# Optimization experiments

Measured on AMD Instinct MI355X. Metric: run time of the kernel, lower is better.

Reference implementation:

```python
import jax, jax.numpy as jnp
import numpy as np

X_DIM, Z_DIM, N_HEIGHT = 256, 256, 32
EPS = 1e-5  # BatchNorm1d eps

def _bn(x, g, b):
    # BatchNorm1d in training mode: batch statistics over the point axis
    m = x.mean(0)
    v = x.var(0)
    return (x - m) * jax.lax.rsqrt(v + EPS) * g + b

def setup_inputs() -> dict:
    key = jax.random.key(0)
    ks = jax.random.split(key, 16)
    B, N, F = 2, 120000, 3
    inp = {
        'pt_fea': jax.random.normal(ks[0], (B, N, F), jnp.float32),
        'grid_ind': jax.random.randint(ks[1], (B, N, 2), 0, 256, dtype=jnp.int32).astype(jnp.int64),
        'occupancy': (jax.random.uniform(ks[2], (B, 1, X_DIM, N_HEIGHT, Z_DIM)) < 0.1).astype(jnp.float32),
    }
    dims = [(3, 64), (64, 128), (128, 256), (256, 512)]
    for i, (di, do) in enumerate(dims):
        inp[f'W{i+1}'] = jax.random.normal(ks[3 + i], (di, do), jnp.float32) * 0.02
        inp[f'b{i+1}'] = jnp.zeros((do,), jnp.float32)
    for i, d in enumerate([3, 64, 128, 256]):
        inp[f'g{i}'] = jnp.ones((d,), jnp.float32)
        inp[f'be{i}'] = jnp.zeros((d,), jnp.float32)
    inp['Wc'] = jax.random.normal(ks[10], (512, 32), jnp.float32) * 0.02
    inp['bc'] = jnp.zeros((32,), jnp.float32)
    return inp

def reference(pt_fea, occupancy, W1, b1, W2, b2, W3, b3, W4, b4,
              g0, be0, g1, be1, g2, be2, g3, be3, Wc, bc, grid_ind):
    B, N, F = pt_fea.shape
    feats = pt_fea.reshape(B * N, F)                          # cat over batch
    # PointNet per-point MLP: BN -> (Linear -> BN -> ReLU) x3 -> Linear
    h = _bn(feats, g0, be0)
    h = jax.nn.relu(_bn(h @ W1 + b1, g1, be1))
    h = jax.nn.relu(_bn(h @ W2 + b2, g2, be2))
    h = jax.nn.relu(_bn(h @ W3 + b3, g3, be3))
    h = h @ W4 + b4                                           # [B*N, 512]

    # linear segment id per (batch, x, z) cell; equivalent to unique+scatter_max
    gi = grid_ind.reshape(B * N, 2).astype(jnp.int32)
    batch_idx = jnp.repeat(jnp.arange(B, dtype=jnp.int32), N)
    seg = batch_idx * (X_DIM * Z_DIM) + gi[:, 0] * Z_DIM + gi[:, 1]
    n_cells = B * X_DIM * Z_DIM

    pooled = jax.ops.segment_max(h, seg, num_segments=n_cells)          # [cells, 512]
    cnt = jax.ops.segment_sum(jnp.ones((B * N,), h.dtype), seg, num_segments=n_cells)
    occ_mask = (cnt > 0)[:, None]
    pooled = jnp.where(occ_mask, pooled, 0.0)                           # kill -inf empties

    # feature compression on occupied cells only; empty cells stay exactly 0
    comp = jax.nn.relu(pooled @ Wc + bc)
    comp = jnp.where(occ_mask, comp, 0.0)                               # [cells, 32]

    bev = comp.reshape(B, X_DIM, Z_DIM, -1).transpose(0, 3, 1, 2)       # [B, 32, X, Z]
    # MaxPool2d(k=3, stride=1, pad=1); -inf padding matches torch's implicit -inf pad
    bev = jax.lax.reduce_window(bev, -jnp.inf, jax.lax.max,
                                (1, 1, 3, 3), (1, 1, 1, 1), 'SAME')

    occu = occupancy[:, 0].transpose(0, 2, 1, 3)                        # [B, H, X, Z]
    out = jnp.concatenate([occu, bev], axis=1)                          # [B, H+32, X, Z]
    return out
```

## Files before the change

### kernel.cpp

```cpp
#include <hip/hip_runtime.h>
#include <hip/hip_bf16.h>

#define EPSN 1e-5f

typedef __bf16 bf16x8 __attribute__((ext_vector_type(8)));
typedef float f32x4 __attribute__((ext_vector_type(4)));

__device__ __forceinline__ unsigned encf(float f) {
  unsigned u = __float_as_uint(f);
  return (u & 0x80000000u) ? ~u : (u | 0x80000000u);
}
__device__ __forceinline__ float decf(unsigned u) {
  return (u & 0x80000000u) ? __uint_as_float(u ^ 0x80000000u) : __uint_as_float(~u);
}

__global__ __launch_bounds__(256) void stats_feats(const float* __restrict__ pt, int n,
                                                   float* __restrict__ sums) {
  float a0 = 0, a1 = 0, a2 = 0, q0 = 0, q1 = 0, q2 = 0;
  for (int p = blockIdx.x * 256 + threadIdx.x; p < n; p += gridDim.x * 256) {
    float v0 = pt[3 * p], v1 = pt[3 * p + 1], v2 = pt[3 * p + 2];
    a0 += v0; a1 += v1; a2 += v2;
    q0 += v0 * v0; q1 += v1 * v1; q2 += v2 * v2;
  }
  __shared__ float red[4][6];
  float vals[6] = {a0, a1, a2, q0, q1, q2};
  int lane = threadIdx.x & 63, wv = threadIdx.x >> 6;
#pragma unroll
  for (int k = 0; k < 6; k++) {
    float v = vals[k];
#pragma unroll
    for (int o = 32; o; o >>= 1) v += __shfl_down(v, o, 64);
    if (lane == 0) red[wv][k] = v;
  }
  __syncthreads();
  if (threadIdx.x < 6) {
    float v = red[0][threadIdx.x] + red[1][threadIdx.x] + red[2][threadIdx.x] + red[3][threadIdx.x];
    atomicAdd(&sums[threadIdx.x], v);
  }
}

__global__ void bn_prep(const float* __restrict__ sums, int C, float invN,
                        const float* __restrict__ g, const float* __restrict__ be,
                        float* __restrict__ sc, float* __restrict__ sh) {
  int c = threadIdx.x;
  if (c < C) {
    float m = sums[c] * invN;
    float v = fmaxf(sums[C + c] * invN - m * m, 0.f);
    float s = g[c] * rsqrtf(v + EPSN);
    sc[c] = s;
    sh[c] = be[c] - m * s;
  }
}

__global__ __launch_bounds__(256) void wconv(const float* __restrict__ W,
                                             __hip_bfloat16* __restrict__ Wt, int K, int C) {
  int idx = blockIdx.x * 256 + threadIdx.x;
  if (idx >= K * C) return;
  int k = idx / C, c = idx - k * C;
  Wt[(size_t)c * K + k] = __float2bfloat16(W[idx]);
}

__global__ __launch_bounds__(256) void gemm1_stats(const float* __restrict__ pt,
                                                   const float* __restrict__ W,
                                                   const float* __restrict__ bias,
                                                   const float* __restrict__ scsh,
                                                   __hip_bfloat16* __restrict__ Y,
                                                   int n, float* __restrict__ sums) {
  const int c = threadIdx.x & 63;
  const float w0 = W[c], w1 = W[64 + c], w2 = W[128 + c], bb = bias[c];
  const float s0 = scsh[0], s1 = scsh[1], s2 = scsh[2];
  const float h0 = scsh[4], h1 = scsh[5], h2 = scsh[6];
  float s = 0.f, q = 0.f;
  const int total = n * 64;
  for (int idx = blockIdx.x * 256 + threadIdx.x; idx < total; idx += gridDim.x * 256) {
    int p = idx >> 6;
    float x0 = s0 * pt[3 * p]     + h0;
    float x1 = s1 * pt[3 * p + 1] + h1;
    float x2 = s2 * pt[3 * p + 2] + h2;
    float y = bb + x0 * w0 + x1 * w1 + x2 * w2;
    Y[idx] = __float2bfloat16(y);
    s += y; q += y * y;
  }
  __shared__ float sred[4][64], qred[4][64];
  int wv = threadIdx.x >> 6;
  sred[wv][c] = s; qred[wv][c] = q;
  __syncthreads();
  if (threadIdx.x < 64) {
    float S = sred[0][c] + sred[1][c] + sred[2][c] + sred[3][c];
    float Q = qred[0][c] + qred[1][c] + qred[2][c] + qred[3][c];
    atomicAdd(&sums[c], S);
    atomicAdd(&sums[64 + c], Q);
  }
}

template <int K>
__global__ __launch_bounds__(256) void gemm_mfma(
    const __hip_bfloat16* __restrict__ Yin, const __hip_bfloat16* __restrict__ Wt,
    const float* __restrict__ bias, const float* __restrict__ sc, const float* __restrict__ sh,
    __hip_bfloat16* __restrict__ Yout, int C, float* __restrict__ sums, int nrows) {
  constexpr int KS = 64, LDA = 72, LDO = 80;
  __shared__ __align__(16) __hip_bfloat16 hA[128 * LDO];
  __shared__ float sredArr[128], qredArr[128];
  const int t = threadIdx.x;
  const int lane = t & 63, wv = t >> 6;
  const int mh = (wv >> 1) * 64, nh = (wv & 1) * 64;
  const int lm = lane & 15, lq = lane >> 4;
  const int p0 = blockIdx.x * 128;
  const int cb0 = blockIdx.y * 128;

  f32x4 acc[4][4];
#pragma unroll
  for (int i = 0; i < 4; i++)
#pragma unroll
    for (int j = 0; j < 4; j++) acc[i][j] = {0.f, 0.f, 0.f, 0.f};

  for (int k0 = 0; k0 < K; k0 += KS) {
    __syncthreads();
#pragma unroll
    for (int it = 0; it < 4; it++) {
      int idx = it * 256 + t;
      int row = idx >> 3;
      int c8 = (idx & 7) * 8;
      int gp = p0 + row;
      __hip_bfloat16 h8[8];
      if (gp < nrows) {
        uint4 raw = *(const uint4*)(Yin + (size_t)gp * K + k0 + c8);
        const __hip_bfloat16* pr = (const __hip_bfloat16*)&raw;
#pragma unroll
        for (int j = 0; j < 8; j++) {
          float v = sc[k0 + c8 + j] * __bfloat162float(pr[j]) + sh[k0 + c8 + j];
          h8[j] = __float2bfloat16(fmaxf(v, 0.f));
        }
      } else {
#pragma unroll
        for (int j = 0; j < 8; j++) h8[j] = __float2bfloat16(0.f);
      }
      *(uint4*)&hA[row * LDA + c8] = *(const uint4*)h8;
    }
    __syncthreads();
#pragma unroll
    for (int kk = 0; kk < KS; kk += 32) {
      bf16x8 a[4], b[4];
#pragma unroll
      for (int i = 0; i < 4; i++)
        a[i] = *(const bf16x8*)&hA[(mh + i * 16 + lm) * LDA + kk + lq * 8];
#pragma unroll
      for (int j = 0; j < 4; j++)
        b[j] = *(const bf16x8*)(const void*)(Wt + (size_t)(cb0 + nh + j * 16 + lm) * K + k0 + kk + lq * 8);
#pragma unroll
      for (int i = 0; i < 4; i++)
#pragma unroll
        for (int j = 0; j < 4; j++)
          acc[i][j] = __builtin_amdgcn_mfma_f32_16x16x32_bf16(a[i], b[j], acc[i][j], 0, 0, 0);
    }
  }

#pragma unroll
  for (int j = 0; j < 4; j++) {
    float bb = bias[cb0 + nh + j * 16 + lm];
#pragma unroll
    for (int i = 0; i < 4; i++)
#pragma unroll
      for (int r = 0; r < 4; r++) acc[i][j][r] += bb;
  }

  __syncthreads();
  if (t < 128) { sredArr[t] = 0.f; qredArr[t] = 0.f; }
  __syncthreads();

#pragma unroll
  for (int j = 0; j < 4; j++) {
    float s = 0.f, q = 0.f;
#pragma unroll
    for (int i = 0; i < 4; i++)
#pragma unroll
      for (int r = 0; r < 4; r++) {
        int grow = p0 + mh + i * 16 + lq * 4 + r;
        if (grow < nrows) { float v = acc[i][j][r]; s += v; q += v * v; }
      }
    s += __shfl_xor(s, 16); s += __shfl_xor(s, 32);
    q += __shfl_xor(q, 16); q += __shfl_xor(q, 32);
    if (lq == 0) {
      atomicAdd(&sredArr[nh + j * 16 + lm], s);
      atomicAdd(&qredArr[nh + j * 16 + lm], q);
    }
  }

  for (int half = 0; half < 2; half++) {
    __syncthreads();
    if ((wv & 1) == half) {
#pragma unroll
      for (int j = 0; j < 4; j++)
#pragma unroll
        for (int i = 0; i < 4; i++)
#pragma unroll
          for (int r = 0; r < 4; r++)
            hA[(mh + i * 16 + lq * 4 + r) * LDO + j * 16 + lm] = __float2bfloat16(acc[i][j][r]);
    }
    __syncthreads();
    int row = t >> 1, seg = t & 1;
    if (p0 + row < nrows) {
      const uint4* src = (const uint4*)&hA[row * LDO + seg * 32];
      uint4* dst = (uint4*)(Yout + (size_t)(p0 + row) * C + cb0 + half * 64 + seg * 32);
      dst[0] = src[0]; dst[1] = src[1]; dst[2] = src[2]; dst[3] = src[3];
    }
  }

  if (t < 128) {
    atomicAdd(&sums[cb0 + t], sredArr[t]);
    atomicAdd(&sums[C + cb0 + t], qredArr[t]);
  }
}

__global__ __launch_bounds__(256) void hist_kernel(const int* __restrict__ gi, int perB,
                                                   unsigned* __restrict__ hist) {
  int b = blockIdx.y;
  int p = blockIdx.x * 256 + threadIdx.x;
  if (p < perB) {
    int gp = b * perB + p;
    int c = (gi[2 * gp] & 255) * 256 + (gi[2 * gp + 1] & 255);
    atomicAdd(&hist[b * 65536 + c], 1u);
  }
}
__global__ __launch_bounds__(256) void scan1(const unsigned* __restrict__ hist,
                                             unsigned* __restrict__ cursor,
                                             unsigned* __restrict__ bSums) {
  __shared__ unsigned s[256];
  int b = blockIdx.y;
  int t = threadIdx.x, i = b * 65536 + blockIdx.x * 256 + t;
  unsigned v = hist[i]; s[t] = v; __syncthreads();
  for (int off = 1; off < 256; off <<= 1) {
    unsigned x = (t >= off) ? s[t - off] : 0u; __syncthreads();
    s[t] += x; __syncthreads();
  }
  cursor[i] = s[t] - v;
  if (t == 255) bSums[b * 256 + blockIdx.x] = s[255];
}
__global__ void scan2(unsigned* __restrict__ bSums) {
  __shared__ unsigned s[256];
  int t = threadIdx.x, i = blockIdx.x * 256 + t;
  unsigned v = bSums[i]; s[t] = v; __syncthreads();
  for (int off = 1; off < 256; off <<= 1) {
    unsigned x = (t >= off) ? s[t - off] : 0u; __syncthreads();
    s[t] += x; __syncthreads();
  }
  bSums[i] = s[t] - v;
}
__global__ __launch_bounds__(256) void mk_starts(const unsigned* __restrict__ cursor,
                                                 const unsigned* __restrict__ bSums,
                                                 unsigned* __restrict__ starts, int perB) {
  int b = blockIdx.y;
  int i = blockIdx.x * 256 + threadIdx.x;
  starts[b * 65537 + i] = cursor[b * 65536 + i] + bSums[b * 256 + (i >> 8)];
  if (i == 0) starts[b * 65537 + 65536] = (unsigned)perB;
}
__global__ __launch_bounds__(256) void scatter_kernel(const int* __restrict__ gi, int perB,
                                                      unsigned* __restrict__ cursor,
                                                      const unsigned* __restrict__ bSums,
                                                      unsigned* __restrict__ sorted,
                                                      unsigned* __restrict__ cells) {
  int b = blockIdx.y;
  int p = blockIdx.x * 256 + threadIdx.x;
  if (p < perB) {
    int gp = b * perB + p;
    int c = (gi[2 * gp] & 255) * 256 + (gi[2 * gp + 1] & 255);
    unsigned pos = atomicAdd(&cursor[b * 65536 + c], 1u) + bSums[b * 256 + (c >> 8)];
    if (pos < (unsigned)perB) {
      sorted[b * perB + pos] = (unsigned)p;
      cells[b * perB + pos] = (unsigned)c;
    }
  }
}

__global__ __launch_bounds__(256, 2) void pool_compress(
    const __hip_bfloat16* __restrict__ Y3, const __hip_bfloat16* __restrict__ Wt4,
    const float* __restrict__ b4, const float* __restrict__ sc, const float* __restrict__ sh,
    const __hip_bfloat16* __restrict__ WcT, const float* __restrict__ bc,
    const unsigned* __restrict__ sortedIdx, const unsigned* __restrict__ sortedCell,
    const unsigned* __restrict__ startsAll, float* __restrict__ comp, int perB) {
  constexpr int K = 256, KS = 64, LDA = 72, MLW = 129, NC = 40;
  __shared__ __align__(16) __hip_bfloat16 hA[128 * LDA];
  __shared__ __align__(16) unsigned maxLds[48 * MLW];
  __shared__ unsigned char slotRow[128];
  __shared__ int rowIdxLds[128];
  const int t = threadIdx.x;
  const int lane = t & 63, wv = t >> 6;
  const int lm = lane & 15, lq = lane >> 4;
  const int mh = (wv >> 1) * 64, nh = (wv & 1) * 64;
  const int batch = blockIdx.y;
  const unsigned* starts = startsAll + batch * 65537;
  const int c0 = blockIdx.x * NC;
  const int cEnd = min(c0 + NC, 65536);
  const int r0 = (int)starts[c0];
  int n = (int)starts[cEnd] - r0;
  if (n > 128) n = 128;
  if (n < 0) n = 0;

  if (t < 128) {
    if (t < n) {
      rowIdxLds[t] = (int)sortedIdx[batch * perB + r0 + t] + batch * perB;
      slotRow[t] = (unsigned char)((sortedCell[batch * perB + r0 + t] - c0) % NC);
    } else {
      rowIdxLds[t] = 0;
      slotRow[t] = 0;
    }
  }

  f32x4 accC[2];
  accC[0] = {0.f, 0.f, 0.f, 0.f};
  accC[1] = {0.f, 0.f, 0.f, 0.f};

#pragma unroll
  for (int half = 0; half < 2; half++) {
    f32x4 acc[2][4][4];
#pragma unroll
    for (int s2 = 0; s2 < 2; s2++)
#pragma unroll
      for (int i = 0; i < 4; i++)
#pragma unroll
        for (int j = 0; j < 4; j++) acc[s2][i][j] = {0.f, 0.f, 0.f, 0.f};

    for (int k0 = 0; k0 < K; k0 += KS) {
      __syncthreads();
#pragma unroll
      for (int it = 0; it < 4; it++) {
        int idx = it * 256 + t;
        int row = idx >> 3;
        int c8 = (idx & 7) * 8;
        __hip_bfloat16 h8[8];
        if (row < n) {
          uint4 raw = *(const uint4*)(Y3 + (size_t)rowIdxLds[row] * K + k0 + c8);
          const __hip_bfloat16* pr = (const __hip_bfloat16*)&raw;
#pragma unroll
          for (int j = 0; j < 8; j++) {
            float v = sc[k0 + c8 + j] * __bfloat162float(pr[j]) + sh[k0 + c8 + j];
            h8[j] = __float2bfloat16(fmaxf(v, 0.f));
          }
        } else {
#pragma unroll
          for (int j = 0; j < 8; j++) h8[j] = __float2bfloat16(0.f);
        }
        *(uint4*)&hA[row * LDA + c8] = *(const uint4*)h8;
      }
      __syncthreads();
#pragma unroll
      for (int kk = 0; kk < KS; kk += 32) {
        bf16x8 a[4];
#pragma unroll
        for (int i = 0; i < 4; i++)
          a[i] = *(const bf16x8*)&hA[(mh + i * 16 + lm) * LDA + kk + lq * 8];
#pragma unroll
        for (int s2 = 0; s2 < 2; s2++) {
          bf16x8 b[4];
#pragma unroll
          for (int j = 0; j < 4; j++)
            b[j] = *(const bf16x8*)(const void*)(Wt4 + (size_t)(half * 256 + s2 * 128 + nh + j * 16 + lm) * K + k0 + kk + lq * 8);
#pragma unroll
          for (int i = 0; i < 4; i++)
#pragma unroll
            for (int j = 0; j < 4; j++)
              acc[s2][i][j] = __builtin_amdgcn_mfma_f32_16x16x32_bf16(a[i], b[j], acc[s2][i][j], 0, 0, 0);
        }
      }
    }

#pragma unroll
    for (int s2 = 0; s2 < 2; s2++) {
      const int cc = half * 2 + s2;
      __syncthreads();
      for (int i = t; i < 48 * MLW; i += 256) maxLds[i] = 0u;
      __syncthreads();
#pragma unroll
      for (int j = 0; j < 4; j++) {
        int colq = nh + j * 16 + lm;
        float bb = b4[cc * 128 + colq];
#pragma unroll
        for (int i = 0; i < 4; i++) {
#pragma unroll
          for (int r = 0; r < 4; r++) {
            int lrow = mh + i * 16 + lq * 4 + r;
            if (lrow < n)
              atomicMax(&maxLds[(int)slotRow[lrow] * MLW + colq], encf(acc[s2][i][j][r] + bb));
          }
        }
      }
      __syncthreads();
      if (wv < 3) {
#pragma unroll
        for (int ks = 0; ks < 4; ks++) {
          int koff = ks * 32 + lq * 8;
          uint4 m0 = *(const uint4*)&maxLds[(wv * 16 + lm) * MLW + koff];
          uint4 m1 = *(const uint4*)&maxLds[(wv * 16 + lm) * MLW + koff + 4];
          unsigned mu[8] = {m0.x, m0.y, m0.z, m0.w, m1.x, m1.y, m1.z, m1.w};
          __hip_bfloat16 af[8];
#pragma unroll
          for (int j = 0; j < 8; j++) af[j] = __float2bfloat16(decf(mu[j]));
          bf16x8 a = *(const bf16x8*)af;
#pragma unroll
          for (int jn = 0; jn < 2; jn++) {
            bf16x8 b = *(const bf16x8*)(const void*)(WcT + (size_t)(jn * 16 + lm) * 512 + cc * 128 + koff);
            accC[jn] = __builtin_amdgcn_mfma_f32_16x16x32_bf16(a, b, accC[jn], 0, 0, 0);
          }
        }
      }
    }
  }
  if (wv < 3) {
#pragma unroll
    for (int jn = 0; jn < 2; jn++) {
      float bb = bc[jn * 16 + lm];
#pragma unroll
      for (int r = 0; r < 4; r++) {
        int cell = c0 + wv * 16 + lq * 4 + r;
        if (cell < cEnd) {
          int occ = starts[cell + 1] > starts[cell];
          float v = occ ? fmaxf(accC[jn][r] + bb, 0.f) : 0.f;
          comp[((size_t)batch * 65536 + cell) * 32 + jn * 16 + lm] = v;
        }
      }
    }
  }
}

__global__ __launch_bounds__(256) void maxpool_write(const float* __restrict__ comp,
                                                     float* __restrict__ out) {
  __shared__ float tile[32][65];
  int bid = blockIdx.x;
  int z0 = (bid & 3) * 64, x = (bid >> 2) & 255, b = bid >> 10;
  int f = threadIdx.x & 31, zs = threadIdx.x >> 5;
  for (int zi = 0; zi < 8; zi++) {
    int z = z0 + zi * 8 + zs;
    float m = -3.402823466e38f;
    for (int dx = -1; dx <= 1; dx++) {
      int xx = x + dx;
      if (xx < 0 || xx > 255) continue;
      for (int dz = -1; dz <= 1; dz++) {
        int zz = z + dz;
        if (zz < 0 || zz > 255) continue;
        m = fmaxf(m, comp[(size_t)((b << 16) + (xx << 8) + zz) * 32 + f]);
      }
    }
    tile[f][zi * 8 + zs] = m;
  }
  __syncthreads();
  int f2 = threadIdx.x >> 3, seg = threadIdx.x & 7;
  float* dst = out + ((size_t)(b * 64 + 32 + f2) * 256 + x) * 256 + z0 + seg * 8;
#pragma unroll
  for (int u = 0; u < 8; u++) dst[u] = tile[f2][seg * 8 + u];
}

__global__ __launch_bounds__(256) void occu_write(const float* __restrict__ occ,
                                                  float* __restrict__ out) {
  int idx = blockIdx.x * 256 + threadIdx.x;
  int z = idx & 255, x = (idx >> 8) & 255, hh = (idx >> 16) & 31, b = idx >> 21;
  out[((size_t)(b * 64 + hh) * 256 + x) * 256 + z] =
      occ[((size_t)((b * 256 + x) * 32 + hh)) * 256 + z];
}

extern "C" void kernel_launch(void* const* d_in, const int* in_sizes, int n_in,
                              void* d_out, int out_size, void* d_ws, size_t ws_size,
                              hipStream_t stream) {
  const float* pt_fea   = (const float*)d_in[0];
  const int*   grid_ind = (const int*)d_in[1];
  const float* occup    = (const float*)d_in[2];
  const float* W1 = (const float*)d_in[3];  const float* b1 = (const float*)d_in[4];
  const float* W2 = (const float*)d_in[5];  const float* b2 = (const float*)d_in[6];
  const float* W3 = (const float*)d_in[7];  const float* b3 = (const float*)d_in[8];
  const float* W4 = (const float*)d_in[9];  const float* b4 = (const float*)d_in[10];
  const float* g0 = (const float*)d_in[11]; const float* be0 = (const float*)d_in[12];
  const float* g1 = (const float*)d_in[13]; const float* be1 = (const float*)d_in[14];
  const float* g2 = (const float*)d_in[15]; const float* be2 = (const float*)d_in[16];
  const float* g3 = (const float*)d_in[17]; const float* be3 = (const float*)d_in[18];
  const float* Wc = (const float*)d_in[19]; const float* bc = (const float*)d_in[20];
  float* out = (float*)d_out;

  const int nPts = in_sizes[0] / 3;
  const int perB = nPts / 2;
  const float invN = 1.f / (float)nPts;

  char* ws = (char*)d_ws;
  float* stats = (float*)ws;
  float* scsh  = (float*)(ws + 4096);
  float* sums0 = stats;        float* sums1 = stats + 16;
  float* sums2 = stats + 160;  float* sums3 = stats + 416;
  float* sc0 = scsh;
  float* sc1 = scsh + 16;   float* sh1 = scsh + 80;
  float* sc2 = scsh + 144;  float* sh2 = scsh + 272;
  float* sc3 = scsh + 400;  float* sh3 = scsh + 656;
  __hip_bfloat16* Wt2 = (__hip_bfloat16*)(ws + 8192);
  __hip_bfloat16* Wt3 = (__hip_bfloat16*)(ws + 24576);
  __hip_bfloat16* Wt4 = (__hip_bfloat16*)(ws + 90112);
  __hip_bfloat16* WcT = (__hip_bfloat16*)(ws + 352256);
  char* S0 = ws + 385024;
  __hip_bfloat16* Y1 = (__hip_bfloat16*)S0;
  __hip_bfloat16* Y2 = (__hip_bfloat16*)(S0 + 30720000ll);
  __hip_bfloat16* Y3 = (__hip_bfloat16*)(S0 + 92160000ll);
  float* comp       = (float*)S0;
  char* sortBase    = S0 + 16777216ll;
  unsigned* hist    = (unsigned*)sortBase;
  unsigned* cursor  = hist + 2 * 65536;
  unsigned* bSums   = cursor + 2 * 65536;
  unsigned* startsA = bSums + 1024;
  unsigned* sorted  = startsA + 131080;
  unsigned* cells   = sorted + 2 * perB;

  hipMemsetAsync(stats, 0, 4096, stream);

  wconv<<<(64 * 128 + 255) / 256, 256, 0, stream>>>(W2, Wt2, 64, 128);
  wconv<<<(128 * 256 + 255) / 256, 256, 0, stream>>>(W3, Wt3, 128, 256);
  wconv<<<(256 * 512 + 255) / 256, 256, 0, stream>>>(W4, Wt4, 256, 512);
  wconv<<<(512 * 32 + 255) / 256, 256, 0, stream>>>(Wc, WcT, 512, 32);

  stats_feats<<<256, 256, 0, stream>>>(pt_fea, nPts, sums0);
  bn_prep<<<1, 256, 0, stream>>>(sums0, 3, invN, g0, be0, sc0, scsh + 4);

  gemm1_stats<<<512, 256, 0, stream>>>(pt_fea, W1, b1, scsh, Y1, nPts, sums1);
  bn_prep<<<1, 256, 0, stream>>>(sums1, 64, invN, g1, be1, sc1, sh1);

  gemm_mfma<64><<<dim3(nPts / 128, 1), 256, 0, stream>>>(Y1, Wt2, b2, sc1, sh1, Y2, 128, sums2, nPts);
  bn_prep<<<1, 256, 0, stream>>>(sums2, 128, invN, g2, be2, sc2, sh2);

  gemm_mfma<128><<<dim3(nPts / 128, 2), 256, 0, stream>>>(Y2, Wt3, b3, sc2, sh2, Y3, 256, sums3, nPts);
  bn_prep<<<1, 256, 0, stream>>>(sums3, 256, invN, g3, be3, sc3, sh3);

  hipMemsetAsync(hist, 0, 2 * 65536 * 4, stream);
  const int pgrid = (perB + 255) / 256;
  hist_kernel<<<dim3(pgrid, 2), 256, 0, stream>>>(grid_ind, perB, hist);
  scan1<<<dim3(256, 2), 256, 0, stream>>>(hist, cursor, bSums);
  scan2<<<2, 256, 0, stream>>>(bSums);
  mk_starts<<<dim3(256, 2), 256, 0, stream>>>(cursor, bSums, startsA, perB);
  scatter_kernel<<<dim3(pgrid, 2), 256, 0, stream>>>(grid_ind, perB, cursor, bSums, sorted, cells);

  pool_compress<<<dim3((65536 + 39) / 40, 2), 256, 0, stream>>>(
      Y3, Wt4, b4, sc3, sh3, WcT, bc, sorted, cells, startsA, comp, perB);

  maxpool_write<<<2048, 256, 0, stream>>>(comp, out);
  occu_write<<<16384, 256, 0, stream>>>(occup, out);
}
```

Before: 830.6 us.

## Sort points by cell before the MLP so pooling reads Y3 contiguously

Moves the counting sort ahead of the MLP. The first layer gathers input points in sorted order, so every later activation buffer is already cell-ordered and pool_compress reads Y3 rows contiguously instead of through an index indirection. Slot assignment is rebuilt from the starts array instead of a per-point cells buffer, MFMA and atomic work is skipped for fully empty 16-row tiles, and the occupancy hint is raised to 3 blocks per CU. The trade-off is a gather in gemm1 and aliasing the sorted buffer into Y2 scratch space, which makes buffer lifetimes more fragile.

```diff
diff --git a/kernel.cpp b/kernel.cpp
--- a/kernel.cpp
+++ b/kernel.cpp
@@ -64,8 +64,9 @@
                                                    const float* __restrict__ W,
                                                    const float* __restrict__ bias,
                                                    const float* __restrict__ scsh,
+                                                   const unsigned* __restrict__ sorted,
                                                    __hip_bfloat16* __restrict__ Y,
-                                                   int n, float* __restrict__ sums) {
+                                                   int n, int perB, float* __restrict__ sums) {
   const int c = threadIdx.x & 63;
   const float w0 = W[c], w1 = W[64 + c], w2 = W[128 + c], bb = bias[c];
   const float s0 = scsh[0], s1 = scsh[1], s2 = scsh[2];
@@ -73,10 +74,11 @@
   float s = 0.f, q = 0.f;
   const int total = n * 64;
   for (int idx = blockIdx.x * 256 + threadIdx.x; idx < total; idx += gridDim.x * 256) {
-    int p = idx >> 6;
-    float x0 = s0 * pt[3 * p]     + h0;
-    float x1 = s1 * pt[3 * p + 1] + h1;
-    float x2 = s2 * pt[3 * p + 2] + h2;
+    int qp = idx >> 6;
+    int orig = (int)sorted[qp] + ((qp >= perB) ? perB : 0);
+    float x0 = s0 * pt[3 * orig]     + h0;
+    float x1 = s1 * pt[3 * orig + 1] + h1;
+    float x2 = s2 * pt[3 * orig + 2] + h2;
     float y = bb + x0 * w0 + x1 * w1 + x2 * w2;
     Y[idx] = __float2bfloat16(y);
     s += y; q += y * y;
@@ -257,32 +259,27 @@
 __global__ __launch_bounds__(256) void scatter_kernel(const int* __restrict__ gi, int perB,
                                                       unsigned* __restrict__ cursor,
                                                       const unsigned* __restrict__ bSums,
-                                                      unsigned* __restrict__ sorted,
-                                                      unsigned* __restrict__ cells) {
+                                                      unsigned* __restrict__ sorted) {
   int b = blockIdx.y;
   int p = blockIdx.x * 256 + threadIdx.x;
   if (p < perB) {
     int gp = b * perB + p;
     int c = (gi[2 * gp] & 255) * 256 + (gi[2 * gp + 1] & 255);
     unsigned pos = atomicAdd(&cursor[b * 65536 + c], 1u) + bSums[b * 256 + (c >> 8)];
-    if (pos < (unsigned)perB) {
+    if (pos < (unsigned)perB)
       sorted[b * perB + pos] = (unsigned)p;
-      cells[b * perB + pos] = (unsigned)c;
-    }
-  }
-}
-
-__global__ __launch_bounds__(256, 2) void pool_compress(
+  }
+}
+
+__global__ __launch_bounds__(256, 3) void pool_compress(
     const __hip_bfloat16* __restrict__ Y3, const __hip_bfloat16* __restrict__ Wt4,
     const float* __restrict__ b4, const float* __restrict__ sc, const float* __restrict__ sh,
     const __hip_bfloat16* __restrict__ WcT, const float* __restrict__ bc,
-    const unsigned* __restrict__ sortedIdx, const unsigned* __restrict__ sortedCell,
     const unsigned* __restrict__ startsAll, float* __restrict__ comp, int perB) {
   constexpr int K = 256, KS = 64, LDA = 72, MLW = 129, NC = 40;
   __shared__ __align__(16) __hip_bfloat16 hA[128 * LDA];
   __shared__ __align__(16) unsigned maxLds[48 * MLW];
   __shared__ unsigned char slotRow[128];
-  __shared__ int rowIdxLds[128];
   const int t = threadIdx.x;
   const int lane = t & 63, wv = t >> 6;
   const int lm = lane & 15, lq = lane >> 4;
@@ -295,15 +292,13 @@
   int n = (int)starts[cEnd] - r0;
   if (n > 128) n = 128;
   if (n < 0) n = 0;
-
-  if (t < 128) {
-    if (t < n) {
-      rowIdxLds[t] = (int)sortedIdx[batch * perB + r0 + t] + batch * perB;
-      slotRow[t] = (unsigned char)((sortedCell[batch * perB + r0 + t] - c0) % NC);
-    } else {
-      rowIdxLds[t] = 0;
-      slotRow[t] = 0;
-    }
+  const size_t rowBase = (size_t)batch * perB + r0;
+
+  if (t < NC && c0 + t < 65536) {
+    int cs = (int)starts[c0 + t] - r0;
+    int ce = (int)starts[c0 + t + 1] - r0;
+    if (ce > 128) ce = 128;
+    for (int i = cs; i < ce; i++) slotRow[i] = (unsigned char)t;
   }
 
   f32x4 accC[2];
@@ -329,7 +324,7 @@
         int c8 = (idx & 7) * 8;
         __hip_bfloat16 h8[8];
         if (row < n) {
-          uint4 raw = *(const uint4*)(Y3 + (size_t)rowIdxLds[row] * K + k0 + c8);
+          uint4 raw = *(const uint4*)(Y3 + (rowBase + row) * K + k0 + c8);
           const __hip_bfloat16* pr = (const __hip_bfloat16*)&raw;
 #pragma unroll
           for (int j = 0; j < 8; j++) {
@@ -348,7 +343,8 @@
         bf16x8 a[4];
 #pragma unroll
         for (int i = 0; i < 4; i++)
-          a[i] = *(const bf16x8*)&hA[(mh + i * 16 + lm) * LDA + kk + lq * 8];
+          if (mh + i * 16 < n)
+            a[i] = *(const bf16x8*)&hA[(mh + i * 16 + lm) * LDA + kk + lq * 8];
 #pragma unroll
         for (int s2 = 0; s2 < 2; s2++) {
           bf16x8 b[4];
@@ -357,9 +353,11 @@
             b[j] = *(const bf16x8*)(const void*)(Wt4 + (size_t)(half * 256 + s2 * 128 + nh + j * 16 + lm) * K + k0 + kk + lq * 8);
 #pragma unroll
           for (int i = 0; i < 4; i++)
-#pragma unroll
-            for (int j = 0; j < 4; j++)
-              acc[s2][i][j] = __builtin_amdgcn_mfma_f32_16x16x32_bf16(a[i], b[j], acc[s2][i][j], 0, 0, 0);
+            if (mh + i * 16 < n) {
+#pragma unroll
+              for (int j = 0; j < 4; j++)
+                acc[s2][i][j] = __builtin_amdgcn_mfma_f32_16x16x32_bf16(a[i], b[j], acc[s2][i][j], 0, 0, 0);
+            }
         }
       }
     }
@@ -376,11 +374,13 @@
         float bb = b4[cc * 128 + colq];
 #pragma unroll
         for (int i = 0; i < 4; i++) {
-#pragma unroll
-          for (int r = 0; r < 4; r++) {
-            int lrow = mh + i * 16 + lq * 4 + r;
-            if (lrow < n)
-              atomicMax(&maxLds[(int)slotRow[lrow] * MLW + colq], encf(acc[s2][i][j][r] + bb));
+          if (mh + i * 16 < n) {
+#pragma unroll
+            for (int r = 0; r < 4; r++) {
+              int lrow = mh + i * 16 + lq * 4 + r;
+              if (lrow < n)
+                atomicMax(&maxLds[(int)slotRow[lrow] * MLW + colq], encf(acc[s2][i][j][r] + bb));
+            }
           }
         }
       }
@@ -495,44 +495,42 @@
   __hip_bfloat16* Y1 = (__hip_bfloat16*)S0;
   __hip_bfloat16* Y2 = (__hip_bfloat16*)(S0 + 30720000ll);
   __hip_bfloat16* Y3 = (__hip_bfloat16*)(S0 + 92160000ll);
-  float* comp       = (float*)S0;
-  char* sortBase    = S0 + 16777216ll;
-  unsigned* hist    = (unsigned*)sortBase;
-  unsigned* cursor  = hist + 2 * 65536;
-  unsigned* bSums   = cursor + 2 * 65536;
-  unsigned* startsA = bSums + 1024;
-  unsigned* sorted  = startsA + 131080;
-  unsigned* cells   = sorted + 2 * perB;
+  unsigned* startsA = (unsigned*)(S0 + 215040000ll);
+  unsigned* hist   = (unsigned*)S0;
+  unsigned* cursor = hist + 2 * 65536;
+  unsigned* bSums  = cursor + 2 * 65536;
+  unsigned* sorted = (unsigned*)Y2;
+  float* comp      = (float*)S0;
 
   hipMemsetAsync(stats, 0, 4096, stream);
+  hipMemsetAsync(hist, 0, 2 * 65536 * 4, stream);
 
   wconv<<<(64 * 128 + 255) / 256, 256, 0, stream>>>(W2, Wt2, 64, 128);
   wconv<<<(128 * 256 + 255) / 256, 256, 0, stream>>>(W3, Wt3, 128, 256);
   wconv<<<(256 * 512 + 255) / 256, 256, 0, stream>>>(W4, Wt4, 256, 512);
   wconv<<<(512 * 32 + 255) / 256, 256, 0, stream>>>(Wc, WcT, 512, 32);
 
-  stats_feats<<<256, 256, 0, stream>>>(pt_fea, nPts, sums0);
-  bn_prep<<<1, 256, 0, stream>>>(sums0, 3, invN, g0, be0, sc0, scsh + 4);
-
-  gemm1_stats<<<512, 256, 0, stream>>>(pt_fea, W1, b1, scsh, Y1, nPts, sums1);
-  bn_prep<<<1, 256, 0, stream>>>(sums1, 64, invN, g1, be1, sc1, sh1);
-
-  gemm_mfma<64><<<dim3(nPts / 128, 1), 256, 0, stream>>>(Y1, Wt2, b2, sc1, sh1, Y2, 128, sums2, nPts);
-  bn_prep<<<1, 256, 0, stream>>>(sums2, 128, invN, g2, be2, sc2, sh2);
-
-  gemm_mfma<128><<<dim3(nPts / 128, 2), 256, 0, stream>>>(Y2, Wt3, b3, sc2, sh2, Y3, 256, sums3, nPts);
-  bn_prep<<<1, 256, 0, stream>>>(sums3, 256, invN, g3, be3, sc3, sh3);
-
-  hipMemsetAsync(hist, 0, 2 * 65536 * 4, stream);
   const int pgrid = (perB + 255) / 256;
   hist_kernel<<<dim3(pgrid, 2), 256, 0, stream>>>(grid_ind, perB, hist);
   scan1<<<dim3(256, 2), 256, 0, stream>>>(hist, cursor, bSums);
   scan2<<<2, 256, 0, stream>>>(bSums);
   mk_starts<<<dim3(256, 2), 256, 0, stream>>>(cursor, bSums, startsA, perB);
-  scatter_kernel<<<dim3(pgrid, 2), 256, 0, stream>>>(grid_ind, perB, cursor, bSums, sorted, cells);
+  scatter_kernel<<<dim3(pgrid, 2), 256, 0, stream>>>(grid_ind, perB, cursor, bSums, sorted);
+
+  stats_feats<<<256, 256, 0, stream>>>(pt_fea, nPts, sums0);
+  bn_prep<<<1, 256, 0, stream>>>(sums0, 3, invN, g0, be0, sc0, scsh + 4);
+
+  gemm1_stats<<<512, 256, 0, stream>>>(pt_fea, W1, b1, scsh, sorted, Y1, nPts, perB, sums1);
+  bn_prep<<<1, 256, 0, stream>>>(sums1, 64, invN, g1, be1, sc1, sh1);
+
+  gemm_mfma<64><<<dim3(nPts / 128, 1), 256, 0, stream>>>(Y1, Wt2, b2, sc1, sh1, Y2, 128, sums2, nPts);
+  bn_prep<<<1, 256, 0, stream>>>(sums2, 128, invN, g2, be2, sc2, sh2);
+
+  gemm_mfma<128><<<dim3(nPts / 128, 2), 256, 0, stream>>>(Y2, Wt3, b3, sc2, sh2, Y3, 256, sums3, nPts);
+  bn_prep<<<1, 256, 0, stream>>>(sums3, 256, invN, g3, be3, sc3, sh3);
 
   pool_compress<<<dim3((65536 + 39) / 40, 2), 256, 0, stream>>>(
-      Y3, Wt4, b4, sc3, sh3, WcT, bc, sorted, cells, startsA, comp, perB);
+      Y3, Wt4, b4, sc3, sh3, WcT, bc, startsA, comp, perB);
 
   maxpool_write<<<2048, 256, 0, stream>>>(comp, out);
   occu_write<<<16384, 256, 0, stream>>>(occup, out);
```

New measurement: 1.211 ms. 1.46x slower.
